# Kernel optimization log

Hardware: AMD Instinct MI355X
Metric: run time of the kernel (lower is better)

Reference implementation:

```python
import jax, jax.numpy as jnp
import numpy as np

SIZE = 4096       # reservoir width
STEPS = 512       # num_steps
BETA = 1.0        # leak factor (LSMNeuron default beta=1.0)
THRESHOLD = 10.0  # LSMNeuron threshold=10

# Heaviside spike with atan surrogate gradient (snntorch default surrogate)
@jax.custom_vjp
def heaviside(x):
    return (x > 0).astype(x.dtype)

def _h_fwd(x):
    return (x > 0).astype(x.dtype), x

def _h_bwd(x, g):
    # snntorch ATan surrogate with alpha=2: d/dx = 1 / (1 + (pi*x)^2)
    return (g / (1.0 + (jnp.pi * x) ** 2),)

heaviside.defvjp(_h_fwd, _h_bwd)


def setup_inputs() -> dict:
    key = jax.random.key(0)
    kx, kw = jax.random.split(key)
    x = jax.random.normal(kx, (STEPS, SIZE), dtype=jnp.float32)
    # fc1 weight: Linear(2*size, size), no bias. Input half | recurrent half.
    W = jax.random.normal(kw, (SIZE, 2 * SIZE), dtype=jnp.float32) / np.sqrt(2 * SIZE)
    return {"x": x, "W": W}


def reference(x, W):
    # Split weight: Wx acts on the external input, Ws on recurrent spikes.
    Wx = W[:, :SIZE]   # [size, size]
    Ws = W[:, SIZE:]   # [size, size]
    # Precompute the input-driven current for all steps as one big GEMM.
    cur_x = jnp.einsum('ts,os->to', x, Wx)  # [steps, size]

    def step(carry, cur_xt):
        spk, mem = carry
        cur = cur_xt + Ws @ spk            # fc1(concat(x[t], spk))
        mem = BETA * mem + cur             # leaky integrate
        spk = heaviside(mem - THRESHOLD)   # fire
        mem = mem - spk * THRESHOLD        # subtract reset
        return (spk, mem), (spk, mem)

    init = (jnp.zeros((SIZE,), jnp.float32), jnp.zeros((SIZE,), jnp.float32))
    _, (spk_rec, mem_rec) = jax.lax.scan(step, init, cur_x)
    # original detaches spk_rec
    return jax.lax.stop_gradient(spk_rec), mem_rec
```

## Files before the change

kernel.cpp:

```cpp
#include <hip/hip_runtime.h>

#define N_SIZE 4096
#define N_STEPS 512
#define WROW 8192
#define THRESH 10.0f

__global__ __launch_bounds__(256) void k_transpose(const float* __restrict__ W,
                                                   float* __restrict__ WsT) {
    __shared__ float tile[32][33];
    const int bs = blockIdx.x * 32;
    const int bo = blockIdx.y * 32;
    const int tx = threadIdx.x;
    const int ty = threadIdx.y;
#pragma unroll
    for (int j = 0; j < 4; ++j)
        tile[ty + j * 8][tx] = W[(size_t)(bo + ty + j * 8) * WROW + N_SIZE + bs + tx];
    __syncthreads();
#pragma unroll
    for (int j = 0; j < 4; ++j)
        WsT[(size_t)(bs + ty + j * 8) * N_SIZE + bo + tx] = tile[tx][ty + j * 8];
}

#define BM 64
#define BN 128
#define BK 16
#define KHALF (N_SIZE / 2)
#define ALD 68
#define BLD 132

#define F4E(v, j) ((j) == 0 ? (v).x : (j) == 1 ? (v).y : (j) == 2 ? (v).z : (v).w)

__global__ __launch_bounds__(128) void k_gemm(const float* __restrict__ x,
                                              const float* __restrict__ W,
                                              float* __restrict__ dst0,
                                              float* __restrict__ dst1) {
    __shared__ float As[BK][ALD];
    __shared__ float Bs[BK][BLD];
    const int tid = threadIdx.x;
    const int bm = blockIdx.y * BM;
    const int bn = blockIdx.x * BN;
    const int kb0 = blockIdx.z * KHALF;
    float* dst = blockIdx.z ? dst1 : dst0;

    const int m0 = (tid >> 4) << 3;
    const int n0 = (tid & 15) << 2;

    const int ar = tid >> 2;
    const int ac = (tid & 3) << 2;
    const float* Ap = &x[(size_t)(bm + ar) * N_SIZE + kb0 + ac];
    const float* Bp = &W[(size_t)(bn + ar) * WROW + kb0 + ac];

    float4 pa0 = *(const float4*)&Ap[0];
    float4 pa1 = *(const float4*)&Ap[(size_t)32 * N_SIZE];
    float4 pb0 = *(const float4*)&Bp[0];
    float4 pb1 = *(const float4*)&Bp[(size_t)32 * WROW];
    float4 pb2 = *(const float4*)&Bp[(size_t)64 * WROW];
    float4 pb3 = *(const float4*)&Bp[(size_t)96 * WROW];

    float acc[8][8];
#pragma unroll
    for (int i = 0; i < 8; ++i)
#pragma unroll
        for (int j = 0; j < 8; ++j) acc[i][j] = 0.f;

    const int nkt = KHALF / BK;
    for (int kt = 0; kt < nkt; ++kt) {
        __syncthreads();
#pragma unroll
        for (int j = 0; j < 4; ++j) {
            As[ac + j][ar]      = F4E(pa0, j);
            As[ac + j][ar + 32] = F4E(pa1, j);
            Bs[ac + j][ar]      = F4E(pb0, j);
            Bs[ac + j][ar + 32] = F4E(pb1, j);
            Bs[ac + j][ar + 64] = F4E(pb2, j);
            Bs[ac + j][ar + 96] = F4E(pb3, j);
        }
        __syncthreads();
        if (kt + 1 < nkt) {
            const float* Ap2 = Ap + (size_t)(kt + 1) * BK;
            const float* Bp2 = Bp + (size_t)(kt + 1) * BK;
            pa0 = *(const float4*)&Ap2[0];
            pa1 = *(const float4*)&Ap2[(size_t)32 * N_SIZE];
            pb0 = *(const float4*)&Bp2[0];
            pb1 = *(const float4*)&Bp2[(size_t)32 * WROW];
            pb2 = *(const float4*)&Bp2[(size_t)64 * WROW];
            pb3 = *(const float4*)&Bp2[(size_t)96 * WROW];
        }
#pragma unroll
        for (int k = 0; k < BK; ++k) {
            const float4 a0 = *(const float4*)&As[k][m0];
            const float4 a1 = *(const float4*)&As[k][m0 + 4];
            const float4 b0 = *(const float4*)&Bs[k][n0];
            const float4 b1 = *(const float4*)&Bs[k][n0 + 64];
            const float av[8] = {a0.x, a0.y, a0.z, a0.w, a1.x, a1.y, a1.z, a1.w};
            const float bv[8] = {b0.x, b0.y, b0.z, b0.w, b1.x, b1.y, b1.z, b1.w};
#pragma unroll
            for (int i = 0; i < 8; ++i)
#pragma unroll
                for (int j = 0; j < 8; ++j)
                    acc[i][j] = fmaf(av[i], bv[j], acc[i][j]);
        }
    }
#pragma unroll
    for (int i = 0; i < 8; ++i) {
        float* cp = &dst[(size_t)(bm + m0 + i) * N_SIZE + bn];
        const float4 o0 = {acc[i][0], acc[i][1], acc[i][2], acc[i][3]};
        const float4 o1 = {acc[i][4], acc[i][5], acc[i][6], acc[i][7]};
        *(float4*)&cp[n0] = o0;
        *(float4*)&cp[n0 + 64] = o1;
    }
}

__global__ __launch_bounds__(256) void k_reduce(float* __restrict__ acc,
                                                const float* __restrict__ part) {
    const size_t i = ((size_t)blockIdx.x * 256 + threadIdx.x) * 4;
    const float4 a = *(const float4*)&acc[i];
    const float4 b = *(const float4*)&part[i];
    const float4 r = {a.x + b.x, a.y + b.y, a.z + b.z, a.w + b.w};
    *(float4*)&acc[i] = r;
}

template <int USE_WST>
__global__ __launch_bounds__(512) void k_scan(const float* __restrict__ WsT,
                                              const float* __restrict__ W,
                                              float* __restrict__ spk_out,
                                              float* __restrict__ mem_out) {
    __shared__ int lst[N_SIZE];
    __shared__ int wcnt[8];
    const int tid = threadIdx.x;
    const int wave = tid >> 6;
    const int lane = tid & 63;
    const int base = tid << 3;
    const unsigned long long below = (lane == 0) ? 0ULL : (~0ULL >> (64 - lane));

    float4 m0 = {0.f, 0.f, 0.f, 0.f}, m1 = {0.f, 0.f, 0.f, 0.f};
    int cnt = 0;

    float4 cn0 = *(const float4*)&mem_out[base];
    float4 cn1 = *(const float4*)&mem_out[base + 4];

    for (int t = 0; t < N_STEPS; ++t) {
        float4 c0 = cn0, c1 = cn1;
        const int tn = (t + 1 < N_STEPS) ? (t + 1) : t;
        const float* nr = &mem_out[(size_t)tn * N_SIZE + base];
        cn0 = *(const float4*)&nr[0];
        cn1 = *(const float4*)&nr[4];

        for (int i = 0; i < cnt; i += 4) {
            const int s0 = lst[i];
            const bool v1 = (i + 1 < cnt), v2 = (i + 2 < cnt), v3 = (i + 3 < cnt);
            const int s1 = v1 ? lst[i + 1] : s0;
            const int s2 = v2 ? lst[i + 2] : s0;
            const int s3 = v3 ? lst[i + 3] : s0;
            const float f1 = v1 ? 1.f : 0.f;
            const float f2 = v2 ? 1.f : 0.f;
            const float f3 = v3 ? 1.f : 0.f;
            float4 w0a, w0b, w1a, w1b, w2a, w2b, w3a, w3b;
            if (USE_WST) {
                const float* p0 = &WsT[(size_t)s0 * N_SIZE + base];
                const float* p1 = &WsT[(size_t)s1 * N_SIZE + base];
                const float* p2 = &WsT[(size_t)s2 * N_SIZE + base];
                const float* p3 = &WsT[(size_t)s3 * N_SIZE + base];
                w0a = *(const float4*)&p0[0]; w0b = *(const float4*)&p0[4];
                w1a = *(const float4*)&p1[0]; w1b = *(const float4*)&p1[4];
                w2a = *(const float4*)&p2[0]; w2b = *(const float4*)&p2[4];
                w3a = *(const float4*)&p3[0]; w3b = *(const float4*)&p3[4];
            } else {
#pragma unroll
                for (int j = 0; j < 4; ++j) {
                    F4E(w0a, j) = W[(size_t)(base + j) * WROW + N_SIZE + s0];
                    F4E(w0b, j) = W[(size_t)(base + 4 + j) * WROW + N_SIZE + s0];
                    F4E(w1a, j) = W[(size_t)(base + j) * WROW + N_SIZE + s1];
                    F4E(w1b, j) = W[(size_t)(base + 4 + j) * WROW + N_SIZE + s1];
                    F4E(w2a, j) = W[(size_t)(base + j) * WROW + N_SIZE + s2];
                    F4E(w2b, j) = W[(size_t)(base + 4 + j) * WROW + N_SIZE + s2];
                    F4E(w3a, j) = W[(size_t)(base + j) * WROW + N_SIZE + s3];
                    F4E(w3b, j) = W[(size_t)(base + 4 + j) * WROW + N_SIZE + s3];
                }
            }
            c0.x += w0a.x; c0.y += w0a.y; c0.z += w0a.z; c0.w += w0a.w;
            c1.x += w0b.x; c1.y += w0b.y; c1.z += w0b.z; c1.w += w0b.w;
            c0.x = fmaf(f1, w1a.x, c0.x); c0.y = fmaf(f1, w1a.y, c0.y);
            c0.z = fmaf(f1, w1a.z, c0.z); c0.w = fmaf(f1, w1a.w, c0.w);
            c1.x = fmaf(f1, w1b.x, c1.x); c1.y = fmaf(f1, w1b.y, c1.y);
            c1.z = fmaf(f1, w1b.z, c1.z); c1.w = fmaf(f1, w1b.w, c1.w);
            c0.x = fmaf(f2, w2a.x, c0.x); c0.y = fmaf(f2, w2a.y, c0.y);
            c0.z = fmaf(f2, w2a.z, c0.z); c0.w = fmaf(f2, w2a.w, c0.w);
            c1.x = fmaf(f2, w2b.x, c1.x); c1.y = fmaf(f2, w2b.y, c1.y);
            c1.z = fmaf(f2, w2b.z, c1.z); c1.w = fmaf(f2, w2b.w, c1.w);
            c0.x = fmaf(f3, w3a.x, c0.x); c0.y = fmaf(f3, w3a.y, c0.y);
            c0.z = fmaf(f3, w3a.z, c0.z); c0.w = fmaf(f3, w3a.w, c0.w);
            c1.x = fmaf(f3, w3b.x, c1.x); c1.y = fmaf(f3, w3b.y, c1.y);
            c1.z = fmaf(f3, w3b.z, c1.z); c1.w = fmaf(f3, w3b.w, c1.w);
        }

        m0.x += c0.x; m0.y += c0.y; m0.z += c0.z; m0.w += c0.w;
        m1.x += c1.x; m1.y += c1.y; m1.z += c1.z; m1.w += c1.w;

        const bool s0b = m0.x > THRESH, s1b = m0.y > THRESH;
        const bool s2b = m0.z > THRESH, s3b = m0.w > THRESH;
        const bool s4b = m1.x > THRESH, s5b = m1.y > THRESH;
        const bool s6b = m1.z > THRESH, s7b = m1.w > THRESH;
        m0.x -= s0b ? THRESH : 0.f;  m0.y -= s1b ? THRESH : 0.f;
        m0.z -= s2b ? THRESH : 0.f;  m0.w -= s3b ? THRESH : 0.f;
        m1.x -= s4b ? THRESH : 0.f;  m1.y -= s5b ? THRESH : 0.f;
        m1.z -= s6b ? THRESH : 0.f;  m1.w -= s7b ? THRESH : 0.f;

        const float4 sp0 = {s0b ? 1.f : 0.f, s1b ? 1.f : 0.f,
                            s2b ? 1.f : 0.f, s3b ? 1.f : 0.f};
        const float4 sp1 = {s4b ? 1.f : 0.f, s5b ? 1.f : 0.f,
                            s6b ? 1.f : 0.f, s7b ? 1.f : 0.f};
        float* srow = &spk_out[(size_t)t * N_SIZE + base];
        float* mrow = &mem_out[(size_t)t * N_SIZE + base];
        *(float4*)&srow[0] = sp0;
        *(float4*)&srow[4] = sp1;
        *(float4*)&mrow[0] = m0;
        *(float4*)&mrow[4] = m1;

        const unsigned long long B0 = __ballot(s0b), B1 = __ballot(s1b);
        const unsigned long long B2 = __ballot(s2b), B3 = __ballot(s3b);
        const unsigned long long B4 = __ballot(s4b), B5 = __ballot(s5b);
        const unsigned long long B6 = __ballot(s6b), B7 = __ballot(s7b);
        const int pre = __popcll(B0 & below) + __popcll(B1 & below) +
                        __popcll(B2 & below) + __popcll(B3 & below) +
                        __popcll(B4 & below) + __popcll(B5 & below) +
                        __popcll(B6 & below) + __popcll(B7 & below);
        if (lane == 0)
            wcnt[wave] = __popcll(B0) + __popcll(B1) + __popcll(B2) + __popcll(B3) +
                         __popcll(B4) + __popcll(B5) + __popcll(B6) + __popcll(B7);
        __syncthreads();

        int woff = 0, total = 0;
#pragma unroll
        for (int w = 0; w < 8; ++w) {
            const int cw = wcnt[w];
            if (w < wave) woff += cw;
            total += cw;
        }
        int off = woff + pre;
        if (s0b) lst[off++] = base + 0;
        if (s1b) lst[off++] = base + 1;
        if (s2b) lst[off++] = base + 2;
        if (s3b) lst[off++] = base + 3;
        if (s4b) lst[off++] = base + 4;
        if (s5b) lst[off++] = base + 5;
        if (s6b) lst[off++] = base + 6;
        if (s7b) lst[off++] = base + 7;
        __syncthreads();

        cnt = total;
    }
}

extern "C" void kernel_launch(void* const* d_in, const int* in_sizes, int n_in,
                              void* d_out, int out_size, void* d_ws, size_t ws_size,
                              hipStream_t stream) {
    const float* x = (const float*)d_in[0];
    const float* W = (const float*)d_in[1];
    float* spk_out = (float*)d_out;
    float* mem_out = spk_out + (size_t)N_STEPS * N_SIZE;
    float* WsT = (float*)d_ws;
    const bool use_wst = ws_size >= (size_t)N_SIZE * N_SIZE * sizeof(float);

    if (use_wst)
        k_transpose<<<dim3(N_SIZE / 32, N_SIZE / 32), dim3(32, 8), 0, stream>>>(W, WsT);

    k_gemm<<<dim3(N_SIZE / BN, N_STEPS / BM, 2), 128, 0, stream>>>(x, W, mem_out, spk_out);
    k_reduce<<<(N_STEPS * N_SIZE) / (256 * 4), 256, 0, stream>>>(mem_out, spk_out);

    if (use_wst)
        k_scan<1><<<1, 512, 0, stream>>>(WsT, W, spk_out, mem_out);
    else
        k_scan<0><<<1, 512, 0, stream>>>(WsT, W, spk_out, mem_out);
}
```

Before: 1.499 ms.

## Split recurrent scan across 16 workgroups with global flag synchronization

Replaces the single-workgroup recurrent scan with a 16-workgroup version. Each workgroup owns 256 neurons and publishes its spike index list plus a step-tagged count into double-buffered global segments. At every step the others poll these with acquire/release atomics, so weight gathers spread over more CUs for more memory-level parallelism. In exchange, each step pays a cross-workgroup polling barrier and a global gather of spike lists, and it relies on all 16 blocks being resident together. The fallback single-block scan is also reworked to 1024 threads with 4 neurons each and a double-buffered list.

```diff
diff --git a/kernel.cpp b/kernel.cpp
--- a/kernel.cpp
+++ b/kernel.cpp
@@ -1,9 +1,18 @@
 #include <hip/hip_runtime.h>
+#include <stdint.h>
 
 #define N_SIZE 4096
 #define N_STEPS 512
 #define WROW 8192
 #define THRESH 10.0f
+
+#define NWG 16
+#define NPW (N_SIZE / NWG)
+#define WST_BYTES ((size_t)N_SIZE * N_SIZE * 4)
+#define SC_UINTS 1024
+#define SEG_INTS (2 * NWG * NPW)
+
+#define F4E(v, j) ((j) == 0 ? (v).x : (j) == 1 ? (v).y : (j) == 2 ? (v).z : (v).w)
 
 __global__ __launch_bounds__(256) void k_transpose(const float* __restrict__ W,
                                                    float* __restrict__ WsT) {
@@ -27,8 +36,6 @@
 #define KHALF (N_SIZE / 2)
 #define ALD 68
 #define BLD 132
-
-#define F4E(v, j) ((j) == 0 ? (v).x : (j) == 1 ? (v).y : (j) == 2 ? (v).z : (v).w)
 
 __global__ __launch_bounds__(128) void k_gemm(const float* __restrict__ x,
                                               const float* __restrict__ W,
@@ -44,7 +51,6 @@
 
     const int m0 = (tid >> 4) << 3;
     const int n0 = (tid & 15) << 2;
-
     const int ar = tid >> 2;
     const int ac = (tid & 3) << 2;
     const float* Ap = &x[(size_t)(bm + ar) * N_SIZE + kb0 + ac];
@@ -120,135 +126,181 @@
     *(float4*)&acc[i] = r;
 }
 
+__global__ __launch_bounds__(256) void k_init(uint32_t* __restrict__ sc) {
+#pragma unroll
+    for (int j = 0; j < SC_UINTS / 256; ++j)
+        sc[j * 256 + threadIdx.x] = 0;
+}
+
+__global__ __launch_bounds__(64) void k_scan_mw(const float* __restrict__ WsT,
+                                                float* __restrict__ spk_out,
+                                                float* __restrict__ mem_out,
+                                                uint32_t* __restrict__ sc,
+                                                int* __restrict__ segs) {
+    __shared__ int list[N_SIZE];
+    __shared__ int cnts[NWG];
+    const int w = blockIdx.x;
+    const int lane = threadIdx.x;
+    const int cb = w * NPW + (lane << 2);
+    const unsigned long long below = (lane == 0) ? 0ULL : (~0ULL >> (64 - lane));
+
+    float4 mem = {0.f, 0.f, 0.f, 0.f};
+    float4 cn = *(const float4*)&mem_out[cb];
+
+    for (int t = 0; t < N_STEPS; ++t) {
+        float4 c = cn;
+
+        int cnt = 0;
+        if (t > 0) {
+            const int par = t & 1;
+            if (lane < NWG) {
+                uint32_t v;
+                for (;;) {
+                    v = __hip_atomic_load(&sc[par * 512 + lane * 32],
+                                          __ATOMIC_ACQUIRE, __HIP_MEMORY_SCOPE_AGENT);
+                    if ((v >> 16) >= (uint32_t)t) break;
+                    __builtin_amdgcn_s_sleep(1);
+                }
+                cnts[lane] = (int)(v & 0xffffu);
+            }
+            __syncthreads();
+            int off[NWG];
+            int tot = 0;
+#pragma unroll
+            for (int u = 0; u < NWG; ++u) { off[u] = tot; tot += cnts[u]; }
+            for (int p = lane; p < tot; p += 64) {
+                int u = 0, o = 0;
+#pragma unroll
+                for (int q = 0; q < NWG; ++q)
+                    if (p >= off[q]) { u = q; o = off[q]; }
+                const int id = __hip_atomic_load(&segs[(par * NWG + u) * NPW + (p - o)],
+                                                 __ATOMIC_RELAXED, __HIP_MEMORY_SCOPE_AGENT);
+                list[p] = id;
+            }
+            __syncthreads();
+            cnt = tot;
+        }
+
+        for (int i = 0; i < cnt; i += 8) {
+            int sx[8];
+            float fx[8];
+#pragma unroll
+            for (int j = 0; j < 8; ++j) {
+                const bool vld = (i + j < cnt);
+                sx[j] = vld ? list[i + j] : list[i];
+                fx[j] = vld ? 1.f : 0.f;
+            }
+            float4 wv[8];
+#pragma unroll
+            for (int j = 0; j < 8; ++j)
+                wv[j] = *(const float4*)&WsT[(size_t)sx[j] * N_SIZE + cb];
+#pragma unroll
+            for (int j = 0; j < 8; ++j) {
+                c.x = fmaf(fx[j], wv[j].x, c.x);
+                c.y = fmaf(fx[j], wv[j].y, c.y);
+                c.z = fmaf(fx[j], wv[j].z, c.z);
+                c.w = fmaf(fx[j], wv[j].w, c.w);
+            }
+        }
+
+        mem.x += c.x; mem.y += c.y; mem.z += c.z; mem.w += c.w;
+        const bool s0 = mem.x > THRESH, s1 = mem.y > THRESH;
+        const bool s2 = mem.z > THRESH, s3 = mem.w > THRESH;
+        mem.x -= s0 ? THRESH : 0.f;  mem.y -= s1 ? THRESH : 0.f;
+        mem.z -= s2 ? THRESH : 0.f;  mem.w -= s3 ? THRESH : 0.f;
+
+        const unsigned long long B0 = __ballot(s0), B1 = __ballot(s1);
+        const unsigned long long B2 = __ballot(s2), B3 = __ballot(s3);
+        const int pre = __popcll(B0 & below) + __popcll(B1 & below) +
+                        __popcll(B2 & below) + __popcll(B3 & below);
+        const int total = __popcll(B0) + __popcll(B1) + __popcll(B2) + __popcll(B3);
+        if (t + 1 < N_STEPS) {
+            const int par2 = (t + 1) & 1;
+            int* myseg = &segs[(par2 * NWG + w) * NPW];
+            int o2 = pre;
+            if (s0) __hip_atomic_store(&myseg[o2++], cb + 0, __ATOMIC_RELAXED, __HIP_MEMORY_SCOPE_AGENT);
+            if (s1) __hip_atomic_store(&myseg[o2++], cb + 1, __ATOMIC_RELAXED, __HIP_MEMORY_SCOPE_AGENT);
+            if (s2) __hip_atomic_store(&myseg[o2++], cb + 2, __ATOMIC_RELAXED, __HIP_MEMORY_SCOPE_AGENT);
+            if (s3) __hip_atomic_store(&myseg[o2++], cb + 3, __ATOMIC_RELAXED, __HIP_MEMORY_SCOPE_AGENT);
+            if (lane == 0)
+                __hip_atomic_store(&sc[par2 * 512 + w * 32],
+                                   ((uint32_t)(t + 1) << 16) | (uint32_t)total,
+                                   __ATOMIC_RELEASE, __HIP_MEMORY_SCOPE_AGENT);
+        }
+
+        const float4 sp = {s0 ? 1.f : 0.f, s1 ? 1.f : 0.f,
+                           s2 ? 1.f : 0.f, s3 ? 1.f : 0.f};
+        *(float4*)&spk_out[(size_t)t * N_SIZE + cb] = sp;
+        *(float4*)&mem_out[(size_t)t * N_SIZE + cb] = mem;
+        const int tn = (t + 1 < N_STEPS) ? (t + 1) : t;
+        cn = *(const float4*)&mem_out[(size_t)tn * N_SIZE + cb];
+    }
+}
+
 template <int USE_WST>
-__global__ __launch_bounds__(512) void k_scan(const float* __restrict__ WsT,
-                                              const float* __restrict__ W,
-                                              float* __restrict__ spk_out,
-                                              float* __restrict__ mem_out) {
-    __shared__ int lst[N_SIZE];
-    __shared__ int wcnt[8];
+__global__ __launch_bounds__(1024) void k_scan1(const float* __restrict__ WsT,
+                                                const float* __restrict__ W,
+                                                float* __restrict__ spk_out,
+                                                float* __restrict__ mem_out) {
+    __shared__ int lists[2][N_SIZE];
+    __shared__ int wcnt[16];
     const int tid = threadIdx.x;
     const int wave = tid >> 6;
     const int lane = tid & 63;
-    const int base = tid << 3;
+    const int base = tid << 2;
     const unsigned long long below = (lane == 0) ? 0ULL : (~0ULL >> (64 - lane));
 
-    float4 m0 = {0.f, 0.f, 0.f, 0.f}, m1 = {0.f, 0.f, 0.f, 0.f};
-    int cnt = 0;
-
-    float4 cn0 = *(const float4*)&mem_out[base];
-    float4 cn1 = *(const float4*)&mem_out[base + 4];
-
+    float4 mem = {0.f, 0.f, 0.f, 0.f};
+    int cnt = 0, cur = 0;
     for (int t = 0; t < N_STEPS; ++t) {
-        float4 c0 = cn0, c1 = cn1;
-        const int tn = (t + 1 < N_STEPS) ? (t + 1) : t;
-        const float* nr = &mem_out[(size_t)tn * N_SIZE + base];
-        cn0 = *(const float4*)&nr[0];
-        cn1 = *(const float4*)&nr[4];
-
-        for (int i = 0; i < cnt; i += 4) {
-            const int s0 = lst[i];
-            const bool v1 = (i + 1 < cnt), v2 = (i + 2 < cnt), v3 = (i + 3 < cnt);
-            const int s1 = v1 ? lst[i + 1] : s0;
-            const int s2 = v2 ? lst[i + 2] : s0;
-            const int s3 = v3 ? lst[i + 3] : s0;
-            const float f1 = v1 ? 1.f : 0.f;
-            const float f2 = v2 ? 1.f : 0.f;
-            const float f3 = v3 ? 1.f : 0.f;
-            float4 w0a, w0b, w1a, w1b, w2a, w2b, w3a, w3b;
+        float* mrow = &mem_out[(size_t)t * N_SIZE + base];
+        float4 c = *(const float4*)mrow;
+        const int* lst = lists[cur];
+        for (int i = 0; i < cnt; ++i) {
+            const int s = lst[i];
+            float4 w0;
             if (USE_WST) {
-                const float* p0 = &WsT[(size_t)s0 * N_SIZE + base];
-                const float* p1 = &WsT[(size_t)s1 * N_SIZE + base];
-                const float* p2 = &WsT[(size_t)s2 * N_SIZE + base];
-                const float* p3 = &WsT[(size_t)s3 * N_SIZE + base];
-                w0a = *(const float4*)&p0[0]; w0b = *(const float4*)&p0[4];
-                w1a = *(const float4*)&p1[0]; w1b = *(const float4*)&p1[4];
-                w2a = *(const float4*)&p2[0]; w2b = *(const float4*)&p2[4];
-                w3a = *(const float4*)&p3[0]; w3b = *(const float4*)&p3[4];
+                w0 = *(const float4*)&WsT[(size_t)s * N_SIZE + base];
             } else {
-#pragma unroll
-                for (int j = 0; j < 4; ++j) {
-                    F4E(w0a, j) = W[(size_t)(base + j) * WROW + N_SIZE + s0];
-                    F4E(w0b, j) = W[(size_t)(base + 4 + j) * WROW + N_SIZE + s0];
-                    F4E(w1a, j) = W[(size_t)(base + j) * WROW + N_SIZE + s1];
-                    F4E(w1b, j) = W[(size_t)(base + 4 + j) * WROW + N_SIZE + s1];
-                    F4E(w2a, j) = W[(size_t)(base + j) * WROW + N_SIZE + s2];
-                    F4E(w2b, j) = W[(size_t)(base + 4 + j) * WROW + N_SIZE + s2];
-                    F4E(w3a, j) = W[(size_t)(base + j) * WROW + N_SIZE + s3];
-                    F4E(w3b, j) = W[(size_t)(base + 4 + j) * WROW + N_SIZE + s3];
-                }
-            }
-            c0.x += w0a.x; c0.y += w0a.y; c0.z += w0a.z; c0.w += w0a.w;
-            c1.x += w0b.x; c1.y += w0b.y; c1.z += w0b.z; c1.w += w0b.w;
-            c0.x = fmaf(f1, w1a.x, c0.x); c0.y = fmaf(f1, w1a.y, c0.y);
-            c0.z = fmaf(f1, w1a.z, c0.z); c0.w = fmaf(f1, w1a.w, c0.w);
-            c1.x = fmaf(f1, w1b.x, c1.x); c1.y = fmaf(f1, w1b.y, c1.y);
-            c1.z = fmaf(f1, w1b.z, c1.z); c1.w = fmaf(f1, w1b.w, c1.w);
-            c0.x = fmaf(f2, w2a.x, c0.x); c0.y = fmaf(f2, w2a.y, c0.y);
-            c0.z = fmaf(f2, w2a.z, c0.z); c0.w = fmaf(f2, w2a.w, c0.w);
-            c1.x = fmaf(f2, w2b.x, c1.x); c1.y = fmaf(f2, w2b.y, c1.y);
-            c1.z = fmaf(f2, w2b.z, c1.z); c1.w = fmaf(f2, w2b.w, c1.w);
-            c0.x = fmaf(f3, w3a.x, c0.x); c0.y = fmaf(f3, w3a.y, c0.y);
-            c0.z = fmaf(f3, w3a.z, c0.z); c0.w = fmaf(f3, w3a.w, c0.w);
-            c1.x = fmaf(f3, w3b.x, c1.x); c1.y = fmaf(f3, w3b.y, c1.y);
-            c1.z = fmaf(f3, w3b.z, c1.z); c1.w = fmaf(f3, w3b.w, c1.w);
-        }
-
-        m0.x += c0.x; m0.y += c0.y; m0.z += c0.z; m0.w += c0.w;
-        m1.x += c1.x; m1.y += c1.y; m1.z += c1.z; m1.w += c1.w;
-
-        const bool s0b = m0.x > THRESH, s1b = m0.y > THRESH;
-        const bool s2b = m0.z > THRESH, s3b = m0.w > THRESH;
-        const bool s4b = m1.x > THRESH, s5b = m1.y > THRESH;
-        const bool s6b = m1.z > THRESH, s7b = m1.w > THRESH;
-        m0.x -= s0b ? THRESH : 0.f;  m0.y -= s1b ? THRESH : 0.f;
-        m0.z -= s2b ? THRESH : 0.f;  m0.w -= s3b ? THRESH : 0.f;
-        m1.x -= s4b ? THRESH : 0.f;  m1.y -= s5b ? THRESH : 0.f;
-        m1.z -= s6b ? THRESH : 0.f;  m1.w -= s7b ? THRESH : 0.f;
-
-        const float4 sp0 = {s0b ? 1.f : 0.f, s1b ? 1.f : 0.f,
-                            s2b ? 1.f : 0.f, s3b ? 1.f : 0.f};
-        const float4 sp1 = {s4b ? 1.f : 0.f, s5b ? 1.f : 0.f,
-                            s6b ? 1.f : 0.f, s7b ? 1.f : 0.f};
-        float* srow = &spk_out[(size_t)t * N_SIZE + base];
-        float* mrow = &mem_out[(size_t)t * N_SIZE + base];
-        *(float4*)&srow[0] = sp0;
-        *(float4*)&srow[4] = sp1;
-        *(float4*)&mrow[0] = m0;
-        *(float4*)&mrow[4] = m1;
-
-        const unsigned long long B0 = __ballot(s0b), B1 = __ballot(s1b);
-        const unsigned long long B2 = __ballot(s2b), B3 = __ballot(s3b);
-        const unsigned long long B4 = __ballot(s4b), B5 = __ballot(s5b);
-        const unsigned long long B6 = __ballot(s6b), B7 = __ballot(s7b);
-        const int pre = __popcll(B0 & below) + __popcll(B1 & below) +
-                        __popcll(B2 & below) + __popcll(B3 & below) +
-                        __popcll(B4 & below) + __popcll(B5 & below) +
-                        __popcll(B6 & below) + __popcll(B7 & below);
+                w0.x = W[(size_t)(base + 0) * WROW + N_SIZE + s];
+                w0.y = W[(size_t)(base + 1) * WROW + N_SIZE + s];
+                w0.z = W[(size_t)(base + 2) * WROW + N_SIZE + s];
+                w0.w = W[(size_t)(base + 3) * WROW + N_SIZE + s];
+            }
+            c.x += w0.x; c.y += w0.y; c.z += w0.z; c.w += w0.w;
+        }
+        mem.x += c.x; mem.y += c.y; mem.z += c.z; mem.w += c.w;
+        const bool s0 = mem.x > THRESH, s1 = mem.y > THRESH;
+        const bool s2 = mem.z > THRESH, s3 = mem.w > THRESH;
+        mem.x -= s0 ? THRESH : 0.f;  mem.y -= s1 ? THRESH : 0.f;
+        mem.z -= s2 ? THRESH : 0.f;  mem.w -= s3 ? THRESH : 0.f;
+        const float4 spkv = {s0 ? 1.f : 0.f, s1 ? 1.f : 0.f,
+                             s2 ? 1.f : 0.f, s3 ? 1.f : 0.f};
+        *(float4*)&spk_out[(size_t)t * N_SIZE + base] = spkv;
+        *(float4*)mrow = mem;
+        const unsigned long long b0 = __ballot(s0), b1 = __ballot(s1);
+        const unsigned long long b2 = __ballot(s2), b3 = __ballot(s3);
+        const int pre = __popcll(b0 & below) + __popcll(b1 & below) +
+                        __popcll(b2 & below) + __popcll(b3 & below);
         if (lane == 0)
-            wcnt[wave] = __popcll(B0) + __popcll(B1) + __popcll(B2) + __popcll(B3) +
-                         __popcll(B4) + __popcll(B5) + __popcll(B6) + __popcll(B7);
+            wcnt[wave] = __popcll(b0) + __popcll(b1) + __popcll(b2) + __popcll(b3);
         __syncthreads();
-
         int woff = 0, total = 0;
 #pragma unroll
-        for (int w = 0; w < 8; ++w) {
-            const int cw = wcnt[w];
-            if (w < wave) woff += cw;
+        for (int wv = 0; wv < 16; ++wv) {
+            const int cw = wcnt[wv];
+            if (wv < wave) woff += cw;
             total += cw;
         }
+        int* nxt = lists[cur ^ 1];
         int off = woff + pre;
-        if (s0b) lst[off++] = base + 0;
-        if (s1b) lst[off++] = base + 1;
-        if (s2b) lst[off++] = base + 2;
-        if (s3b) lst[off++] = base + 3;
-        if (s4b) lst[off++] = base + 4;
-        if (s5b) lst[off++] = base + 5;
-        if (s6b) lst[off++] = base + 6;
-        if (s7b) lst[off++] = base + 7;
+        if (s0) nxt[off++] = base;
+        if (s1) nxt[off++] = base + 1;
+        if (s2) nxt[off++] = base + 2;
+        if (s3) nxt[off++] = base + 3;
         __syncthreads();
-
         cnt = total;
+        cur ^= 1;
     }
 }
 
@@ -260,7 +312,10 @@
     float* spk_out = (float*)d_out;
     float* mem_out = spk_out + (size_t)N_STEPS * N_SIZE;
     float* WsT = (float*)d_ws;
-    const bool use_wst = ws_size >= (size_t)N_SIZE * N_SIZE * sizeof(float);
+    uint32_t* sc = (uint32_t*)((char*)d_ws + WST_BYTES);
+    int* segs = (int*)((char*)d_ws + WST_BYTES + SC_UINTS * 4);
+    const bool use_wst = ws_size >= WST_BYTES;
+    const bool mw = ws_size >= WST_BYTES + SC_UINTS * 4 + SEG_INTS * 4;
 
     if (use_wst)
         k_transpose<<<dim3(N_SIZE / 32, N_SIZE / 32), dim3(32, 8), 0, stream>>>(W, WsT);
@@ -268,8 +323,12 @@
     k_gemm<<<dim3(N_SIZE / BN, N_STEPS / BM, 2), 128, 0, stream>>>(x, W, mem_out, spk_out);
     k_reduce<<<(N_STEPS * N_SIZE) / (256 * 4), 256, 0, stream>>>(mem_out, spk_out);
 
-    if (use_wst)
-        k_scan<1><<<1, 512, 0, stream>>>(WsT, W, spk_out, mem_out);
-    else
-        k_scan<0><<<1, 512, 0, stream>>>(WsT, W, spk_out, mem_out);
-}
+    if (mw) {
+        k_init<<<1, 256, 0, stream>>>(sc);
+        k_scan_mw<<<NWG, 64, 0, stream>>>(WsT, spk_out, mem_out, sc, segs);
+    } else if (use_wst) {
+        k_scan1<1><<<1, 1024, 0, stream>>>(WsT, W, spk_out, mem_out);
+    } else {
+        k_scan1<0><<<1, 1024, 0, stream>>>(WsT, W, spk_out, mem_out);
+    }
+}
```

New measurement: 1.667 ms. 11.2% more time.

## Pad spike list with zero-row sentinel and unroll gather by twelve in scan

Applied to the files above, without the earlier changes.

Adds a zero row after the transposed recurrent weights and pads the spike index list with sentinel entries pointing to it. The scan can then gather twelve weight columns per iteration with no validity masks, using readfirstlane to keep indices scalar. The next step's input loads and the output stores move before the barrier, and the scan is split into two launches that hand off state through workspace. Fallback paths use a new 1024-thread kernel with double-buffered lists. This trades extra padded loads and an extra launch for more memory-level parallelism in the serial scan.

```diff
diff --git a/kernel.cpp b/kernel.cpp
--- a/kernel.cpp
+++ b/kernel.cpp
@@ -1,9 +1,19 @@
 #include <hip/hip_runtime.h>
+#include <stdint.h>
 
 #define N_SIZE 4096
 #define N_STEPS 512
 #define WROW 8192
 #define THRESH 10.0f
+#define CCAP 12
+
+#define WST_BYTES ((size_t)(N_SIZE + 1) * N_SIZE * 4)
+#define SMEM_OFF  WST_BYTES
+#define SLST_OFF  (WST_BYTES + (size_t)N_SIZE * 4)
+#define FULL_WS   (SLST_OFF + (size_t)(N_SIZE + 17) * 4)
+
+#define F4E(v, j) ((j) == 0 ? (v).x : (j) == 1 ? (v).y : (j) == 2 ? (v).z : (v).w)
+#define ADD4(a, b) { (a).x += (b).x; (a).y += (b).y; (a).z += (b).z; (a).w += (b).w; }
 
 __global__ __launch_bounds__(256) void k_transpose(const float* __restrict__ W,
                                                    float* __restrict__ WsT) {
@@ -21,14 +31,16 @@
         WsT[(size_t)(bs + ty + j * 8) * N_SIZE + bo + tx] = tile[tx][ty + j * 8];
 }
 
+__global__ __launch_bounds__(256) void k_zero_row(float* __restrict__ WsT) {
+    WsT[(size_t)N_SIZE * N_SIZE + blockIdx.x * 256 + threadIdx.x] = 0.f;
+}
+
 #define BM 64
 #define BN 128
 #define BK 16
 #define KHALF (N_SIZE / 2)
 #define ALD 68
 #define BLD 132
-
-#define F4E(v, j) ((j) == 0 ? (v).x : (j) == 1 ? (v).y : (j) == 2 ? (v).z : (v).w)
 
 __global__ __launch_bounds__(128) void k_gemm(const float* __restrict__ x,
                                               const float* __restrict__ W,
@@ -44,7 +56,6 @@
 
     const int m0 = (tid >> 4) << 3;
     const int n0 = (tid & 15) << 2;
-
     const int ar = tid >> 2;
     const int ac = (tid & 3) << 2;
     const float* Ap = &x[(size_t)(bm + ar) * N_SIZE + kb0 + ac];
@@ -120,12 +131,17 @@
     *(float4*)&acc[i] = r;
 }
 
-template <int USE_WST>
-__global__ __launch_bounds__(512) void k_scan(const float* __restrict__ WsT,
-                                              const float* __restrict__ W,
-                                              float* __restrict__ spk_out,
-                                              float* __restrict__ mem_out) {
-    __shared__ int lst[N_SIZE];
+#define GCOL(k)                                                               \
+    const int s##k = __builtin_amdgcn_readfirstlane(lst[n0 + k]);             \
+    const float* p##k = &WsT[(size_t)s##k * N_SIZE + base];
+
+__global__ __launch_bounds__(512) void k_scanF(const float* __restrict__ WsT,
+                                               float* __restrict__ spk_out,
+                                               float* __restrict__ mem_out,
+                                               float* __restrict__ smem,
+                                               int* __restrict__ slst,
+                                               int t0, int t1) {
+    __shared__ int lst[N_SIZE + 16];
     __shared__ int wcnt[8];
     const int tid = threadIdx.x;
     const int wave = tid >> 6;
@@ -134,69 +150,52 @@
     const unsigned long long below = (lane == 0) ? 0ULL : (~0ULL >> (64 - lane));
 
     float4 m0 = {0.f, 0.f, 0.f, 0.f}, m1 = {0.f, 0.f, 0.f, 0.f};
-    int cnt = 0;
-
-    float4 cn0 = *(const float4*)&mem_out[base];
-    float4 cn1 = *(const float4*)&mem_out[base + 4];
-
-    for (int t = 0; t < N_STEPS; ++t) {
+    int tot = 0;
+
+    if (t0 != 0) {
+        m0 = *(const float4*)&smem[base];
+        m1 = *(const float4*)&smem[base + 4];
+        for (int i = tid; i < N_SIZE + 16; i += 512) lst[i] = slst[i];
+        tot = slst[N_SIZE + 16];
+        __syncthreads();
+    }
+
+    float4 cn0 = *(const float4*)&mem_out[(size_t)t0 * N_SIZE + base];
+    float4 cn1 = *(const float4*)&mem_out[(size_t)t0 * N_SIZE + base + 4];
+
+    for (int t = t0; t < t1; ++t) {
         float4 c0 = cn0, c1 = cn1;
-        const int tn = (t + 1 < N_STEPS) ? (t + 1) : t;
-        const float* nr = &mem_out[(size_t)tn * N_SIZE + base];
-        cn0 = *(const float4*)&nr[0];
-        cn1 = *(const float4*)&nr[4];
-
-        for (int i = 0; i < cnt; i += 4) {
-            const int s0 = lst[i];
-            const bool v1 = (i + 1 < cnt), v2 = (i + 2 < cnt), v3 = (i + 3 < cnt);
-            const int s1 = v1 ? lst[i + 1] : s0;
-            const int s2 = v2 ? lst[i + 2] : s0;
-            const int s3 = v3 ? lst[i + 3] : s0;
-            const float f1 = v1 ? 1.f : 0.f;
-            const float f2 = v2 ? 1.f : 0.f;
-            const float f3 = v3 ? 1.f : 0.f;
-            float4 w0a, w0b, w1a, w1b, w2a, w2b, w3a, w3b;
-            if (USE_WST) {
-                const float* p0 = &WsT[(size_t)s0 * N_SIZE + base];
-                const float* p1 = &WsT[(size_t)s1 * N_SIZE + base];
-                const float* p2 = &WsT[(size_t)s2 * N_SIZE + base];
-                const float* p3 = &WsT[(size_t)s3 * N_SIZE + base];
-                w0a = *(const float4*)&p0[0]; w0b = *(const float4*)&p0[4];
-                w1a = *(const float4*)&p1[0]; w1b = *(const float4*)&p1[4];
-                w2a = *(const float4*)&p2[0]; w2b = *(const float4*)&p2[4];
-                w3a = *(const float4*)&p3[0]; w3b = *(const float4*)&p3[4];
-            } else {
-#pragma unroll
-                for (int j = 0; j < 4; ++j) {
-                    F4E(w0a, j) = W[(size_t)(base + j) * WROW + N_SIZE + s0];
-                    F4E(w0b, j) = W[(size_t)(base + 4 + j) * WROW + N_SIZE + s0];
-                    F4E(w1a, j) = W[(size_t)(base + j) * WROW + N_SIZE + s1];
-                    F4E(w1b, j) = W[(size_t)(base + 4 + j) * WROW + N_SIZE + s1];
-                    F4E(w2a, j) = W[(size_t)(base + j) * WROW + N_SIZE + s2];
-                    F4E(w2b, j) = W[(size_t)(base + 4 + j) * WROW + N_SIZE + s2];
-                    F4E(w3a, j) = W[(size_t)(base + j) * WROW + N_SIZE + s3];
-                    F4E(w3b, j) = W[(size_t)(base + 4 + j) * WROW + N_SIZE + s3];
-                }
-            }
-            c0.x += w0a.x; c0.y += w0a.y; c0.z += w0a.z; c0.w += w0a.w;
-            c1.x += w0b.x; c1.y += w0b.y; c1.z += w0b.z; c1.w += w0b.w;
-            c0.x = fmaf(f1, w1a.x, c0.x); c0.y = fmaf(f1, w1a.y, c0.y);
-            c0.z = fmaf(f1, w1a.z, c0.z); c0.w = fmaf(f1, w1a.w, c0.w);
-            c1.x = fmaf(f1, w1b.x, c1.x); c1.y = fmaf(f1, w1b.y, c1.y);
-            c1.z = fmaf(f1, w1b.z, c1.z); c1.w = fmaf(f1, w1b.w, c1.w);
-            c0.x = fmaf(f2, w2a.x, c0.x); c0.y = fmaf(f2, w2a.y, c0.y);
-            c0.z = fmaf(f2, w2a.z, c0.z); c0.w = fmaf(f2, w2a.w, c0.w);
-            c1.x = fmaf(f2, w2b.x, c1.x); c1.y = fmaf(f2, w2b.y, c1.y);
-            c1.z = fmaf(f2, w2b.z, c1.z); c1.w = fmaf(f2, w2b.w, c1.w);
-            c0.x = fmaf(f3, w3a.x, c0.x); c0.y = fmaf(f3, w3a.y, c0.y);
-            c0.z = fmaf(f3, w3a.z, c0.z); c0.w = fmaf(f3, w3a.w, c0.w);
-            c1.x = fmaf(f3, w3b.x, c1.x); c1.y = fmaf(f3, w3b.y, c1.y);
-            c1.z = fmaf(f3, w3b.z, c1.z); c1.w = fmaf(f3, w3b.w, c1.w);
-        }
-
-        m0.x += c0.x; m0.y += c0.y; m0.z += c0.z; m0.w += c0.w;
-        m1.x += c1.x; m1.y += c1.y; m1.z += c1.z; m1.w += c1.w;
-
+
+        for (int n0 = 0; n0 < tot; n0 += CCAP) {
+            GCOL(0)  GCOL(1)  GCOL(2)  GCOL(3)  GCOL(4)  GCOL(5)
+            GCOL(6)  GCOL(7)  GCOL(8)  GCOL(9)  GCOL(10) GCOL(11)
+            const float4 a0 = *(const float4*)&p0[0],  b0v = *(const float4*)&p0[4];
+            const float4 a1 = *(const float4*)&p1[0],  b1v = *(const float4*)&p1[4];
+            const float4 a2 = *(const float4*)&p2[0],  b2v = *(const float4*)&p2[4];
+            const float4 a3 = *(const float4*)&p3[0],  b3v = *(const float4*)&p3[4];
+            const float4 a4 = *(const float4*)&p4[0],  b4v = *(const float4*)&p4[4];
+            const float4 a5 = *(const float4*)&p5[0],  b5v = *(const float4*)&p5[4];
+            const float4 a6 = *(const float4*)&p6[0],  b6v = *(const float4*)&p6[4];
+            const float4 a7 = *(const float4*)&p7[0],  b7v = *(const float4*)&p7[4];
+            const float4 a8 = *(const float4*)&p8[0],  b8v = *(const float4*)&p8[4];
+            const float4 a9 = *(const float4*)&p9[0],  b9v = *(const float4*)&p9[4];
+            const float4 aA = *(const float4*)&p10[0], bAv = *(const float4*)&p10[4];
+            const float4 aB = *(const float4*)&p11[0], bBv = *(const float4*)&p11[4];
+            ADD4(c0, a0) ADD4(c1, b0v)
+            ADD4(c0, a1) ADD4(c1, b1v)
+            ADD4(c0, a2) ADD4(c1, b2v)
+            ADD4(c0, a3) ADD4(c1, b3v)
+            ADD4(c0, a4) ADD4(c1, b4v)
+            ADD4(c0, a5) ADD4(c1, b5v)
+            ADD4(c0, a6) ADD4(c1, b6v)
+            ADD4(c0, a7) ADD4(c1, b7v)
+            ADD4(c0, a8) ADD4(c1, b8v)
+            ADD4(c0, a9) ADD4(c1, b9v)
+            ADD4(c0, aA) ADD4(c1, bAv)
+            ADD4(c0, aB) ADD4(c1, bBv)
+        }
+
+        ADD4(m0, c0) ADD4(m1, c1)
         const bool s0b = m0.x > THRESH, s1b = m0.y > THRESH;
         const bool s2b = m0.z > THRESH, s3b = m0.w > THRESH;
         const bool s4b = m1.x > THRESH, s5b = m1.y > THRESH;
@@ -205,17 +204,6 @@
         m0.z -= s2b ? THRESH : 0.f;  m0.w -= s3b ? THRESH : 0.f;
         m1.x -= s4b ? THRESH : 0.f;  m1.y -= s5b ? THRESH : 0.f;
         m1.z -= s6b ? THRESH : 0.f;  m1.w -= s7b ? THRESH : 0.f;
-
-        const float4 sp0 = {s0b ? 1.f : 0.f, s1b ? 1.f : 0.f,
-                            s2b ? 1.f : 0.f, s3b ? 1.f : 0.f};
-        const float4 sp1 = {s4b ? 1.f : 0.f, s5b ? 1.f : 0.f,
-                            s6b ? 1.f : 0.f, s7b ? 1.f : 0.f};
-        float* srow = &spk_out[(size_t)t * N_SIZE + base];
-        float* mrow = &mem_out[(size_t)t * N_SIZE + base];
-        *(float4*)&srow[0] = sp0;
-        *(float4*)&srow[4] = sp1;
-        *(float4*)&mrow[0] = m0;
-        *(float4*)&mrow[4] = m1;
 
         const unsigned long long B0 = __ballot(s0b), B1 = __ballot(s1b);
         const unsigned long long B2 = __ballot(s2b), B3 = __ballot(s3b);
@@ -228,14 +216,29 @@
         if (lane == 0)
             wcnt[wave] = __popcll(B0) + __popcll(B1) + __popcll(B2) + __popcll(B3) +
                          __popcll(B4) + __popcll(B5) + __popcll(B6) + __popcll(B7);
-        __syncthreads();
-
-        int woff = 0, total = 0;
+
+        const float4 sp0 = {s0b ? 1.f : 0.f, s1b ? 1.f : 0.f,
+                            s2b ? 1.f : 0.f, s3b ? 1.f : 0.f};
+        const float4 sp1 = {s4b ? 1.f : 0.f, s5b ? 1.f : 0.f,
+                            s6b ? 1.f : 0.f, s7b ? 1.f : 0.f};
+        float* srow = &spk_out[(size_t)t * N_SIZE + base];
+        float* mrow = &mem_out[(size_t)t * N_SIZE + base];
+        *(float4*)&srow[0] = sp0;
+        *(float4*)&srow[4] = sp1;
+        *(float4*)&mrow[0] = m0;
+        *(float4*)&mrow[4] = m1;
+        const int tn = (t + 1 < N_STEPS) ? (t + 1) : t;
+        cn0 = *(const float4*)&mem_out[(size_t)tn * N_SIZE + base];
+        cn1 = *(const float4*)&mem_out[(size_t)tn * N_SIZE + base + 4];
+
+        __syncthreads();
+
+        int woff = 0, tt = 0;
 #pragma unroll
         for (int w = 0; w < 8; ++w) {
             const int cw = wcnt[w];
             if (w < wave) woff += cw;
-            total += cw;
+            tt += cw;
         }
         int off = woff + pre;
         if (s0b) lst[off++] = base + 0;
@@ -246,9 +249,84 @@
         if (s5b) lst[off++] = base + 5;
         if (s6b) lst[off++] = base + 6;
         if (s7b) lst[off++] = base + 7;
-        __syncthreads();
-
+        if (tid < 16) lst[tt + tid] = N_SIZE;
+        __syncthreads();
+
+        tot = tt;
+    }
+
+    if (t1 < N_STEPS) {
+        *(float4*)&smem[base] = m0;
+        *(float4*)&smem[base + 4] = m1;
+        for (int i = tid; i < N_SIZE + 16; i += 512) slst[i] = lst[i];
+        if (tid == 0) slst[N_SIZE + 16] = tot;
+    }
+}
+
+template <int USE_WST>
+__global__ __launch_bounds__(1024) void k_scan1(const float* __restrict__ WsT,
+                                                const float* __restrict__ W,
+                                                float* __restrict__ spk_out,
+                                                float* __restrict__ mem_out) {
+    __shared__ int lists[2][N_SIZE];
+    __shared__ int wcnt[16];
+    const int tid = threadIdx.x;
+    const int wave = tid >> 6;
+    const int lane = tid & 63;
+    const int base = tid << 2;
+    const unsigned long long below = (lane == 0) ? 0ULL : (~0ULL >> (64 - lane));
+
+    float4 mem = {0.f, 0.f, 0.f, 0.f};
+    int cnt = 0, cur = 0;
+    for (int t = 0; t < N_STEPS; ++t) {
+        float* mrow = &mem_out[(size_t)t * N_SIZE + base];
+        float4 c = *(const float4*)mrow;
+        const int* lstp = lists[cur];
+        for (int i = 0; i < cnt; ++i) {
+            const int s = lstp[i];
+            float4 w0;
+            if (USE_WST) {
+                w0 = *(const float4*)&WsT[(size_t)s * N_SIZE + base];
+            } else {
+                w0.x = W[(size_t)(base + 0) * WROW + N_SIZE + s];
+                w0.y = W[(size_t)(base + 1) * WROW + N_SIZE + s];
+                w0.z = W[(size_t)(base + 2) * WROW + N_SIZE + s];
+                w0.w = W[(size_t)(base + 3) * WROW + N_SIZE + s];
+            }
+            ADD4(c, w0)
+        }
+        ADD4(mem, c)
+        const bool s0 = mem.x > THRESH, s1 = mem.y > THRESH;
+        const bool s2 = mem.z > THRESH, s3 = mem.w > THRESH;
+        mem.x -= s0 ? THRESH : 0.f;  mem.y -= s1 ? THRESH : 0.f;
+        mem.z -= s2 ? THRESH : 0.f;  mem.w -= s3 ? THRESH : 0.f;
+        const float4 spkv = {s0 ? 1.f : 0.f, s1 ? 1.f : 0.f,
+                             s2 ? 1.f : 0.f, s3 ? 1.f : 0.f};
+        *(float4*)&spk_out[(size_t)t * N_SIZE + base] = spkv;
+        *(float4*)mrow = mem;
+        const unsigned long long b0 = __ballot(s0), b1 = __ballot(s1);
+        const unsigned long long b2 = __ballot(s2), b3 = __ballot(s3);
+        const int pre = __popcll(b0 & below) + __popcll(b1 & below) +
+                        __popcll(b2 & below) + __popcll(b3 & below);
+        if (lane == 0)
+            wcnt[wave] = __popcll(b0) + __popcll(b1) + __popcll(b2) + __popcll(b3);
+        __syncthreads();
+        int woff = 0, total = 0;
+#pragma unroll
+        for (int wv = 0; wv < 16; ++wv) {
+            const int cw = wcnt[wv];
+            if (wv < wave) woff += cw;
+            total += cw;
+        }
+        int* nxt = lists[cur ^ 1];
+        int off = woff + pre;
+        if (s0) nxt[off++] = base;
+        if (s1) nxt[off++] = base + 1;
+        if (s2) nxt[off++] = base + 2;
+        if (s3) nxt[off++] = base + 3;
+        __syncthreads();
         cnt = total;
+        cur ^= 1;
     }
 }
 
@@ -260,16 +338,27 @@
     float* spk_out = (float*)d_out;
     float* mem_out = spk_out + (size_t)N_STEPS * N_SIZE;
     float* WsT = (float*)d_ws;
-    const bool use_wst = ws_size >= (size_t)N_SIZE * N_SIZE * sizeof(float);
-
-    if (use_wst)
+    float* smem = (float*)((char*)d_ws + SMEM_OFF);
+    int* slst = (int*)((char*)d_ws + SLST_OFF);
+    const bool full = ws_size >= FULL_WS;
+    const bool use_wst = ws_size >= (size_t)N_SIZE * N_SIZE * 4;
+
+    if (full) {
+        k_zero_row<<<16, 256, 0, stream>>>(WsT);
         k_transpose<<<dim3(N_SIZE / 32, N_SIZE / 32), dim3(32, 8), 0, stream>>>(W, WsT);
+    } else if (use_wst) {
+        k_transpose<<<dim3(N_SIZE / 32, N_SIZE / 32), dim3(32, 8), 0, stream>>>(W, WsT);
+    }
 
     k_gemm<<<dim3(N_SIZE / BN, N_STEPS / BM, 2), 128, 0, stream>>>(x, W, mem_out, spk_out);
     k_reduce<<<(N_STEPS * N_SIZE) / (256 * 4), 256, 0, stream>>>(mem_out, spk_out);
 
-    if (use_wst)
-        k_scan<1><<<1, 512, 0, stream>>>(WsT, W, spk_out, mem_out);
-    else
-        k_scan<0><<<1, 512, 0, stream>>>(WsT, W, spk_out, mem_out);
-}
+    if (full) {
+        k_scanF<<<1, 512, 0, stream>>>(WsT, spk_out, mem_out, smem, slst, 0, 256);
+        k_scanF<<<1, 512, 0, stream>>>(WsT, spk_out, mem_out, smem, slst, 256, 512);
+    } else if (use_wst) {
+        k_scan1<1><<<1, 1024, 0, stream>>>(WsT, W, spk_out, mem_out);
+    } else {
+        k_scan1<0><<<1, 1024, 0, stream>>>(WsT, W, spk_out, mem_out);
+    }
+}
```

New measurement: 1.811 ms. 1.21x slower.
